# Performance work log

Hardware: AMD Instinct MI355X
Metric: run time of the kernel (lower is better)

## Reference

```python
import jax, jax.numpy as jnp
import numpy as np

N = 100000   # nodes
E = 1600000  # edges
IN = 32      # in_channels
ED = 16      # edge_dim
G = 128      # num graphs in batch
NEG = 0.01   # LeakyReLU default slope

def lrelu(v):
    return jnp.where(v > 0, v, NEG * v)

def gine_conv(x, src, dst, edge_attr, We, be, Wa, ba, Wb, bb):
    # PyG GINEConv (eps=0): out = nn(x + sum_{j->i} relu(x_j + lin(edge_attr)))
    e = edge_attr @ We + be                      # [E, d]
    m = jax.nn.relu(x[src] + e)                  # gather + add + relu
    agg = jax.ops.segment_sum(m, dst, num_segments=x.shape[0])
    h = x + agg
    return lrelu(h @ Wa + ba) @ Wb + bb

def setup_inputs() -> dict:
    key = jax.random.key(0)
    ks = jax.random.split(key, 24)
    w = lambda k, shape: (jax.random.normal(k, shape, dtype=jnp.float32) * 0.05)
    inp = {
        "x": jax.random.normal(ks[0], (N, IN), dtype=jnp.float32),
        "edge_index": jax.random.randint(ks[1], (2, E), 0, N),
        "edge_attr": jax.random.normal(ks[2], (E, ED), dtype=jnp.float32),
        "batch": jnp.sort(jax.random.randint(ks[3], (N,), 0, G)),
        # conv1: edge lin ED->IN, nn IN->32->64
        "We1": w(ks[4], (ED, IN)), "be1": w(ks[5], (IN,)),
        "W1a": w(ks[6], (IN, 32)), "b1a": w(ks[7], (32,)),
        "W1b": w(ks[8], (32, 64)), "b1b": w(ks[9], (64,)),
        # conv2: edge lin ED->64, nn 64->128->256
        "We2": w(ks[10], (ED, 64)), "be2": w(ks[11], (64,)),
        "W2a": w(ks[12], (64, 128)), "b2a": w(ks[13], (128,)),
        "W2b": w(ks[14], (128, 256)), "b2b": w(ks[15], (256,)),
        # head
        "Wf0": w(ks[16], (256, 128)), "bf0": w(ks[17], (128,)),
        "Wf1": w(ks[18], (128, 64)), "bf1": w(ks[19], (64,)),
        "Wf2": w(ks[20], (64, 32)), "bf2": w(ks[21], (32,)),
        "Wr": w(ks[22], (32, 1)), "br": w(ks[23], (1,)),
    }
    return inp

def reference(x, edge_index, edge_attr, batch,
              We1, be1, W1a, b1a, W1b, b1b,
              We2, be2, W2a, b2a, W2b, b2b,
              Wf0, bf0, Wf1, bf1, Wf2, bf2, Wr, br):
    src, dst = edge_index[0], edge_index[1]
    h = gine_conv(x, src, dst, edge_attr, We1, be1, W1a, b1a, W1b, b1b)
    h = lrelu(h)
    h = gine_conv(h, src, dst, edge_attr, We2, be2, W2a, b2a, W2b, b2b)
    h = lrelu(h)
    # global_add_pool over graph ids
    g = jax.ops.segment_sum(h, batch, num_segments=G)   # [G, 256]
    g = lrelu(g @ Wf0 + bf0)
    # dropout: identity (inference reference)
    g = lrelu(g @ Wf1 + bf1)
    g = lrelu(g @ Wf2 + bf2)
    out = (g @ Wr + br)[:, 0]                           # squeeze(dim=1)
    return out
```

## Files before the change

### kernel.cpp

```cpp
#include <hip/hip_runtime.h>

__device__ __forceinline__ float lrelu(float v){ return v > 0.f ? v : 0.01f*v; }

typedef __attribute__((ext_vector_type(8))) short v8s;
typedef __attribute__((ext_vector_type(4))) float v4f;

__device__ __forceinline__ unsigned short f2bf(float f){
    union{float f; unsigned int i;} v; v.f = f;
    unsigned int u = v.i;
    return (unsigned short)((u + 0x7fffu + ((u >> 16) & 1u)) >> 16);
}
__device__ __forceinline__ unsigned int pack2(float a, float b){
    return (unsigned int)f2bf(a) | ((unsigned int)f2bf(b) << 16);
}
__device__ __forceinline__ float bflo(unsigned int u){
    union{unsigned int i; float f;} v; v.i = u << 16; return v.f;
}
__device__ __forceinline__ float bfhi(unsigned int u){
    union{unsigned int i; float f;} v; v.i = u & 0xffff0000u; return v.f;
}
__device__ __forceinline__ float bf2f(unsigned short s){
    union{unsigned int i; float f;} v; v.i = ((unsigned int)s) << 16; return v.f;
}

__global__ __launch_bounds__(256) void k_hist(
    const int* __restrict__ ei, int* __restrict__ deg, int E)
{
    int e = blockIdx.x * 256 + threadIdx.x;
    if (e >= E) return;
    atomicAdd(&deg[ei[E + e]], 1);
}

__global__ __launch_bounds__(256) void k_scan1(
    const int* __restrict__ deg, int* __restrict__ rowptr,
    int* __restrict__ bsum, int N)
{
    __shared__ int sh[256];
    int t = threadIdx.x;
    int i = blockIdx.x * 256 + t;
    int v = (i < N) ? deg[i] : 0;
    sh[t] = v;
    __syncthreads();
    #pragma unroll
    for (int off = 1; off < 256; off <<= 1) {
        int add = (t >= off) ? sh[t - off] : 0;
        __syncthreads();
        sh[t] += add;
        __syncthreads();
    }
    if (i < N) rowptr[i] = sh[t] - v;
    if (t == 255) bsum[blockIdx.x] = sh[t];
}

__global__ __launch_bounds__(512) void k_scan2(int* __restrict__ bsum, int nb)
{
    __shared__ int sh[512];
    int t = threadIdx.x;
    int v = (t < nb) ? bsum[t] : 0;
    sh[t] = v;
    __syncthreads();
    #pragma unroll
    for (int off = 1; off < 512; off <<= 1) {
        int add = (t >= off) ? sh[t - off] : 0;
        __syncthreads();
        sh[t] += add;
        __syncthreads();
    }
    if (t < nb) bsum[t] = sh[t] - v;
}

__global__ __launch_bounds__(256) void k_scan3(
    int* __restrict__ rowptr, int* __restrict__ cursor,
    const int* __restrict__ bsum, int N)
{
    int i = blockIdx.x * 256 + threadIdx.x;
    if (i >= N) return;
    int rp = rowptr[i] + bsum[i >> 8];
    rowptr[i] = rp;
    cursor[i] = rp;
}

__global__ __launch_bounds__(256) void k_castx(
    const float* __restrict__ x, unsigned int* __restrict__ xb, int M8)
{
    int i = blockIdx.x * 256 + threadIdx.x;
    if (i >= M8) return;
    const float4* p = reinterpret_cast<const float4*>(x) + (size_t)i * 2;
    float4 a = p[0], b = p[1];
    uint4 o;
    o.x = pack2(a.x, a.y); o.y = pack2(a.z, a.w);
    o.z = pack2(b.x, b.y); o.w = pack2(b.z, b.w);
    reinterpret_cast<uint4*>(xb)[i] = o;
}

__global__ __launch_bounds__(256) void k_castw(
    const float* __restrict__ W2a, const float* __restrict__ W2b,
    unsigned short* __restrict__ W2aT, unsigned short* __restrict__ W2bT)
{
    int i = blockIdx.x * 256 + threadIdx.x;
    if (i < 128 * 64) {
        int n = i >> 6, k = i & 63;
        W2aT[i] = f2bf(W2a[k * 128 + n]);
    }
    int j = i - 128 * 64;
    if (j >= 0 && j < 256 * 128) {
        int n = j >> 7, k = j & 127;
        W2bT[j] = f2bf(W2b[k * 256 + n]);
    }
}

__global__ __launch_bounds__(256) void k_scatter(
    const int* __restrict__ ei, const float* __restrict__ ea,
    int* __restrict__ cursor, int2* __restrict__ csr2,
    uint4* __restrict__ eab, int E)
{
    int e = blockIdx.x * 256 + threadIdx.x;
    if (e >= E) return;
    int s = ei[e];
    int d = ei[E + e];
    int slot = atomicAdd(&cursor[d], 1);
    const float4* p = reinterpret_cast<const float4*>(ea) + (size_t)e * 4;
    float4 a = p[0], b = p[1], c = p[2], f = p[3];
    uint4 o0, o1;
    o0.x = pack2(a.x, a.y); o0.y = pack2(a.z, a.w);
    o0.z = pack2(b.x, b.y); o0.w = pack2(b.z, b.w);
    o1.x = pack2(c.x, c.y); o1.y = pack2(c.z, c.w);
    o1.z = pack2(f.x, f.y); o1.w = pack2(f.z, f.w);
    eab[(size_t)slot * 2]     = o0;
    eab[(size_t)slot * 2 + 1] = o1;
    int2 r; r.x = s; r.y = d;
    csr2[slot] = r;
}

__device__ __forceinline__ void edge_mlp(
    const uint4& A0, const uint4& A1,
    const float (&w0)[16], const float (&w1)[16],
    float b0, float b1, unsigned int hv,
    float& acc0, float& acc1)
{
    float m0 = b0, m1 = b1, f;
    f = bflo(A0.x); m0 = fmaf(f, w0[0],  m0); m1 = fmaf(f, w1[0],  m1);
    f = bfhi(A0.x); m0 = fmaf(f, w0[1],  m0); m1 = fmaf(f, w1[1],  m1);
    f = bflo(A0.y); m0 = fmaf(f, w0[2],  m0); m1 = fmaf(f, w1[2],  m1);
    f = bfhi(A0.y); m0 = fmaf(f, w0[3],  m0); m1 = fmaf(f, w1[3],  m1);
    f = bflo(A0.z); m0 = fmaf(f, w0[4],  m0); m1 = fmaf(f, w1[4],  m1);
    f = bfhi(A0.z); m0 = fmaf(f, w0[5],  m0); m1 = fmaf(f, w1[5],  m1);
    f = bflo(A0.w); m0 = fmaf(f, w0[6],  m0); m1 = fmaf(f, w1[6],  m1);
    f = bfhi(A0.w); m0 = fmaf(f, w0[7],  m0); m1 = fmaf(f, w1[7],  m1);
    f = bflo(A1.x); m0 = fmaf(f, w0[8],  m0); m1 = fmaf(f, w1[8],  m1);
    f = bfhi(A1.x); m0 = fmaf(f, w0[9],  m0); m1 = fmaf(f, w1[9],  m1);
    f = bflo(A1.y); m0 = fmaf(f, w0[10], m0); m1 = fmaf(f, w1[10], m1);
    f = bfhi(A1.y); m0 = fmaf(f, w0[11], m0); m1 = fmaf(f, w1[11], m1);
    f = bflo(A1.z); m0 = fmaf(f, w0[12], m0); m1 = fmaf(f, w1[12], m1);
    f = bfhi(A1.z); m0 = fmaf(f, w0[13], m0); m1 = fmaf(f, w1[13], m1);
    f = bflo(A1.w); m0 = fmaf(f, w0[14], m0); m1 = fmaf(f, w1[14], m1);
    f = bfhi(A1.w); m0 = fmaf(f, w0[15], m0); m1 = fmaf(f, w1[15], m1);
    m0 += bflo(hv); m1 += bfhi(hv);
    acc0 += (m0 > 0.f ? m0 : 0.f);
    acc1 += (m1 > 0.f ? m1 : 0.f);
}

#define SPW1 128
#define CHL1 32
__global__ __launch_bounds__(256) void k_agg1(
    const unsigned int* __restrict__ xb, const uint4* __restrict__ eab,
    const float* __restrict__ We, const float* __restrict__ be,
    const int2* __restrict__ csr2, float* __restrict__ agg, int E)
{
    const int tid = threadIdx.x;
    const int c2 = tid & 15;
    const int chain = (tid >> 4) & 3;
    const int wave = __builtin_amdgcn_readfirstlane((blockIdx.x * 256 + tid) >> 6);
    const int s0 = wave * SPW1 + chain * CHL1;
    if (s0 >= E) return;
    const int n = (s0 + CHL1 <= E) ? CHL1 : E - s0;
    const int n1 = n - 1;

    float w0[16], w1[16];
    #pragma unroll
    for (int k = 0; k < 16; ++k) {
        w0[k] = We[k * 32 + 2 * c2];
        w1[k] = We[k * 32 + 2 * c2 + 1];
    }
    const float bias0 = be[2 * c2], bias1 = be[2 * c2 + 1];

    const int2* cp = csr2 + s0;
    const uint4* ep = eab + (size_t)s0 * 2;

    int j1 = (1 <= n1) ? 1 : n1;
    int j2 = (2 <= n1) ? 2 : n1;
    int2 r0 = cp[0];
    int2 r1 = cp[j1];
    int2 r2 = cp[j2];
    unsigned int h0  = xb[(unsigned)r0.x * 16 + c2];
    unsigned int h1v = xb[(unsigned)r1.x * 16 + c2];
    uint4 a0 = ep[0],      a1 = ep[1];
    uint4 b0 = ep[2 * j1], b1 = ep[2 * j1 + 1];

    int cur = r0.y;
    bool owned = false;
    float acc0 = 0.f, acc1 = 0.f;

    #pragma unroll 2
    for (int i = 0; i < n; ++i) {
        int i3 = (i + 3 <= n1) ? i + 3 : n1;
        int2 r3 = cp[i3];
        int i2 = (i + 2 <= n1) ? i + 2 : n1;
        unsigned int h2 = xb[(unsigned)r2.x * 16 + c2];
        uint4 c0 = ep[2 * i2], c1 = ep[2 * i2 + 1];

        if (r0.y != cur) {
            if (owned) {
                float2 v; v.x = acc0; v.y = acc1;
                *reinterpret_cast<float2*>(&agg[(unsigned)cur * 32 + 2 * c2]) = v;
            } else {
                atomicAdd(&agg[(unsigned)cur * 32 + 2 * c2],     acc0);
                atomicAdd(&agg[(unsigned)cur * 32 + 2 * c2 + 1], acc1);
            }
            acc0 = acc1 = 0.f; cur = r0.y; owned = true;
        }
        edge_mlp(a0, a1, w0, w1, bias0, bias1, h0, acc0, acc1);
        r0 = r1; r1 = r2; r2 = r3;
        h0 = h1v; h1v = h2;
        a0 = b0; a1 = b1; b0 = c0; b1 = c1;
    }
    atomicAdd(&agg[(unsigned)cur * 32 + 2 * c2],     acc0);
    atomicAdd(&agg[(unsigned)cur * 32 + 2 * c2 + 1], acc1);
}

#define SPW2 64
#define CHL2 32
__global__ __launch_bounds__(256) void k_agg2(
    const unsigned int* __restrict__ h1b, const uint4* __restrict__ eab,
    const float* __restrict__ We, const float* __restrict__ be,
    const int2* __restrict__ csr2, float* __restrict__ agg, int E)
{
    const int tid = threadIdx.x;
    const int c2 = tid & 31;
    const int chain = (tid >> 5) & 1;
    const int wave = __builtin_amdgcn_readfirstlane((blockIdx.x * 256 + tid) >> 6);
    const int s0 = wave * SPW2 + chain * CHL2;
    if (s0 >= E) return;
    const int n = (s0 + CHL2 <= E) ? CHL2 : E - s0;
    const int n1 = n - 1;

    float w0[16], w1[16];
    #pragma unroll
    for (int k = 0; k < 16; ++k) {
        w0[k] = We[k * 64 + 2 * c2];
        w1[k] = We[k * 64 + 2 * c2 + 1];
    }
    const float bias0 = be[2 * c2], bias1 = be[2 * c2 + 1];

    const int2* cp = csr2 + s0;
    const uint4* ep = eab + (size_t)s0 * 2;

    int j1 = (1 <= n1) ? 1 : n1;
    int j2 = (2 <= n1) ? 2 : n1;
    int2 r0 = cp[0];
    int2 r1 = cp[j1];
    int2 r2 = cp[j2];
    unsigned int h0  = h1b[(unsigned)r0.x * 32 + c2];
    unsigned int h1v = h1b[(unsigned)r1.x * 32 + c2];
    uint4 a0 = ep[0],      a1 = ep[1];
    uint4 b0 = ep[2 * j1], b1 = ep[2 * j1 + 1];

    int cur = r0.y;
    bool owned = false;
    float acc0 = 0.f, acc1 = 0.f;

    #pragma unroll 2
    for (int i = 0; i < n; ++i) {
        int i3 = (i + 3 <= n1) ? i + 3 : n1;
        int2 r3 = cp[i3];
        int i2 = (i + 2 <= n1) ? i + 2 : n1;
        unsigned int h2 = h1b[(unsigned)r2.x * 32 + c2];
        uint4 c0 = ep[2 * i2], c1 = ep[2 * i2 + 1];

        if (r0.y != cur) {
            if (owned) {
                float2 v; v.x = acc0; v.y = acc1;
                *reinterpret_cast<float2*>(&agg[(unsigned)cur * 64 + 2 * c2]) = v;
            } else {
                atomicAdd(&agg[(unsigned)cur * 64 + 2 * c2],     acc0);
                atomicAdd(&agg[(unsigned)cur * 64 + 2 * c2 + 1], acc1);
            }
            acc0 = acc1 = 0.f; cur = r0.y; owned = true;
        }
        edge_mlp(a0, a1, w0, w1, bias0, bias1, h0, acc0, acc1);
        r0 = r1; r1 = r2; r2 = r3;
        h0 = h1v; h1v = h2;
        a0 = b0; a1 = b1; b0 = c0; b1 = c1;
    }
    atomicAdd(&agg[(unsigned)cur * 64 + 2 * c2],     acc0);
    atomicAdd(&agg[(unsigned)cur * 64 + 2 * c2 + 1], acc1);
}

__global__ __launch_bounds__(256, 4) void k_mlp1(
    const float* __restrict__ x, const float* __restrict__ agg1,
    const float* __restrict__ W1a, const float* __restrict__ b1a,
    const float* __restrict__ W1b, const float* __restrict__ b1b,
    float* __restrict__ h1, unsigned int* __restrict__ h1b, int N)
{
    __shared__ float ts[64][33];
    const int tid = threadIdx.x;
    const int n0 = blockIdx.x * 64;
    const int row = tid & 63;
    const int grp = __builtin_amdgcn_readfirstlane(tid >> 6);
    const int g = n0 + row;

    float hv[32];
    if (g < N) {
        const float4* xp = reinterpret_cast<const float4*>(x) + (size_t)g * 8;
        const float4* ap = reinterpret_cast<const float4*>(agg1) + (size_t)g * 8;
        #pragma unroll
        for (int q = 0; q < 8; ++q) {
            float4 a = xp[q], b = ap[q];
            hv[4*q+0]=a.x+b.x; hv[4*q+1]=a.y+b.y;
            hv[4*q+2]=a.z+b.z; hv[4*q+3]=a.w+b.w;
        }
    } else {
        #pragma unroll
        for (int q = 0; q < 32; ++q) hv[q] = 0.f;
    }

    {
        const int c0 = grp * 8;
        float acc[8];
        #pragma unroll
        for (int i = 0; i < 8; ++i) acc[i] = b1a[c0 + i];
        for (int k = 0; k < 32; ++k) {
            float h = hv[k];
            const float* w = W1a + k*32 + c0;
            #pragma unroll
            for (int i = 0; i < 8; ++i) acc[i] = fmaf(h, w[i], acc[i]);
        }
        #pragma unroll
        for (int i = 0; i < 8; ++i) ts[row][c0 + i] = lrelu(acc[i]);
    }
    __syncthreads();

    {
        const int c0 = grp * 16;
        float acc[16];
        #pragma unroll
        for (int i = 0; i < 16; ++i) acc[i] = b1b[c0 + i];
        for (int k = 0; k < 32; ++k) {
            float tv = ts[row][k];
            const float* w = W1b + k*64 + c0;
            #pragma unroll
            for (int i = 0; i < 16; ++i) acc[i] = fmaf(tv, w[i], acc[i]);
        }
        if (g < N) {
            #pragma unroll
            for (int i = 0; i < 16; ++i) acc[i] = lrelu(acc[i]);
            float4* op = reinterpret_cast<float4*>(h1) + (size_t)g*16 + (c0>>2);
            #pragma unroll
            for (int q = 0; q < 4; ++q) {
                float4 o;
                o.x = acc[4*q+0]; o.y = acc[4*q+1];
                o.z = acc[4*q+2]; o.w = acc[4*q+3];
                op[q] = o;
            }
            uint4 p0, p1;
            p0.x = pack2(acc[0],  acc[1]);  p0.y = pack2(acc[2],  acc[3]);
            p0.z = pack2(acc[4],  acc[5]);  p0.w = pack2(acc[6],  acc[7]);
            p1.x = pack2(acc[8],  acc[9]);  p1.y = pack2(acc[10], acc[11]);
            p1.z = pack2(acc[12], acc[13]); p1.w = pack2(acc[14], acc[15]);
            uint4* bp = reinterpret_cast<uint4*>(h1b + (size_t)g*32 + (c0>>1));
            bp[0] = p0; bp[1] = p1;
        }
    }
}

__global__ __launch_bounds__(256) void k_mlp2(
    const float* __restrict__ h1, const float* __restrict__ agg2,
    const unsigned short* __restrict__ W2aT, const float* __restrict__ b2a,
    const unsigned short* __restrict__ W2bT, const float* __restrict__ b2b,
    unsigned short* __restrict__ h2b, int N)
{
    __shared__ unsigned short hs[64][72];
    __shared__ unsigned short ts[64][136];
    const int tid = threadIdx.x;
    const int n0 = blockIdx.x * 64;

    {
        int r = tid >> 2, cseg = (tid & 3) * 16;
        int g = n0 + r;
        uint4 o0 = {0,0,0,0}, o1 = {0,0,0,0};
        if (g < N) {
            const float4* xp = reinterpret_cast<const float4*>(h1)
                               + (size_t)g*16 + (cseg>>2);
            const float4* ap = reinterpret_cast<const float4*>(agg2)
                               + (size_t)g*16 + (cseg>>2);
            float4 a0=xp[0], a1=xp[1], a2=xp[2], a3=xp[3];
            float4 b0=ap[0], b1=ap[1], b2=ap[2], b3=ap[3];
            o0.x = pack2(a0.x+b0.x, a0.y+b0.y); o0.y = pack2(a0.z+b0.z, a0.w+b0.w);
            o0.z = pack2(a1.x+b1.x, a1.y+b1.y); o0.w = pack2(a1.z+b1.z, a1.w+b1.w);
            o1.x = pack2(a2.x+b2.x, a2.y+b2.y); o1.y = pack2(a2.z+b2.z, a2.w+b2.w);
            o1.z = pack2(a3.x+b3.x, a3.y+b3.y); o1.w = pack2(a3.z+b3.z, a3.w+b3.w);
        }
        uint4* dp = reinterpret_cast<uint4*>(&hs[r][cseg]);
        dp[0] = o0; dp[1] = o1;
    }
    __syncthreads();

    const int wv   = __builtin_amdgcn_readfirstlane(tid >> 6);
    const int lane = tid & 63;
    const int lid  = lane & 15;
    const int quad = lane >> 4;

    v8s afA0 = *reinterpret_cast<const v8s*>(&hs[wv*16 + lid][quad*8]);
    v8s afA1 = *reinterpret_cast<const v8s*>(&hs[wv*16 + lid][32 + quad*8]);
    #pragma unroll
    for (int nt = 0; nt < 8; ++nt) {
        v4f acc = {0.f, 0.f, 0.f, 0.f};
        const unsigned short* wp = W2aT + (nt*16 + lid)*64 + quad*8;
        v8s b0 = *reinterpret_cast<const v8s*>(wp);
        v8s b1 = *reinterpret_cast<const v8s*>(wp + 32);
        acc = __builtin_amdgcn_mfma_f32_16x16x32_bf16(afA0, b0, acc, 0, 0, 0);
        acc = __builtin_amdgcn_mfma_f32_16x16x32_bf16(afA1, b1, acc, 0, 0, 0);
        float bias = b2a[nt*16 + lid];
        #pragma unroll
        for (int i = 0; i < 4; ++i) {
            float v = lrelu(acc[i] + bias);
            ts[wv*16 + quad*4 + i][nt*16 + lid] = f2bf(v);
        }
    }
    __syncthreads();

    v8s afB[4];
    #pragma unroll
    for (int ks = 0; ks < 4; ++ks)
        afB[ks] = *reinterpret_cast<const v8s*>(&ts[wv*16 + lid][ks*32 + quad*8]);
    const int gbase = n0 + wv*16 + quad*4;
    #pragma unroll 4
    for (int nt = 0; nt < 16; ++nt) {
        v4f acc = {0.f, 0.f, 0.f, 0.f};
        const unsigned short* wp = W2bT + (nt*16 + lid)*128 + quad*8;
        #pragma unroll
        for (int ks = 0; ks < 4; ++ks) {
            v8s bf = *reinterpret_cast<const v8s*>(wp + ks*32);
            acc = __builtin_amdgcn_mfma_f32_16x16x32_bf16(afB[ks], bf, acc, 0, 0, 0);
        }
        float bias = b2b[nt*16 + lid];
        #pragma unroll
        for (int i = 0; i < 4; ++i) {
            int g = gbase + i;
            if (g < N) {
                float v = lrelu(acc[i] + bias);
                h2b[(size_t)g*256 + nt*16 + lid] = f2bf(v);
            }
        }
    }
}

__global__ __launch_bounds__(256) void k_pool(
    const unsigned int* __restrict__ h2b, const int* __restrict__ batch,
    float* __restrict__ g, int N)
{
    int tid = threadIdx.x;
    int c2 = tid & 127;
    int h = tid >> 7;
    int base = blockIdx.x * 128;
    int n0 = base + h;
    int nend = base + 128; if (nend > N) nend = N;
    if (n0 >= N) return;
    float acc0 = 0.f, acc1 = 0.f;
    int cur = batch[n0];
    for (int n = n0; n < nend; n += 2) {
        int b = batch[n];
        unsigned int hv = h2b[(size_t)n * 128 + c2];
        if (b != cur) {
            atomicAdd(&g[(unsigned)cur * 256 + 2*c2],     acc0);
            atomicAdd(&g[(unsigned)cur * 256 + 2*c2 + 1], acc1);
            acc0 = acc1 = 0.f; cur = b;
        }
        acc0 += bflo(hv); acc1 += bfhi(hv);
    }
    atomicAdd(&g[(unsigned)cur * 256 + 2*c2],     acc0);
    atomicAdd(&g[(unsigned)cur * 256 + 2*c2 + 1], acc1);
}

__global__ __launch_bounds__(256) void k_head(
    const float* __restrict__ g,
    const float* __restrict__ Wf0, const float* __restrict__ bf0,
    const float* __restrict__ Wf1, const float* __restrict__ bf1,
    const float* __restrict__ Wf2, const float* __restrict__ bf2,
    const float* __restrict__ Wr,  const float* __restrict__ br,
    float* __restrict__ out)
{
    __shared__ float buf[256];
    __shared__ float t0[128];
    __shared__ float t1[64];
    __shared__ float t2[32];
    int gid = blockIdx.x, tid = threadIdx.x;
    buf[tid] = g[(size_t)gid*256 + tid];
    __syncthreads();
    if (tid < 128) {
        float acc = bf0[tid];
        for (int k = 0; k < 256; ++k) acc = fmaf(buf[k], Wf0[k*128 + tid], acc);
        t0[tid] = lrelu(acc);
    }
    __syncthreads();
    if (tid < 64) {
        float acc = bf1[tid];
        for (int k = 0; k < 128; ++k) acc = fmaf(t0[k], Wf1[k*64 + tid], acc);
        t1[tid] = lrelu(acc);
    }
    __syncthreads();
    if (tid < 32) {
        float acc = bf2[tid];
        for (int k = 0; k < 64; ++k) acc = fmaf(t1[k], Wf2[k*32 + tid], acc);
        t2[tid] = lrelu(acc);
    }
    __syncthreads();
    if (tid == 0) {
        float acc = br[0];
        for (int k = 0; k < 32; ++k) acc = fmaf(t2[k], Wr[k], acc);
        out[gid] = acc;
    }
}

extern "C" void kernel_launch(void* const* d_in, const int* in_sizes, int n_in,
                              void* d_out, int out_size, void* d_ws, size_t ws_size,
                              hipStream_t stream)
{
    const float* x     = (const float*)d_in[0];
    const int*   ei    = (const int*)d_in[1];
    const float* ea    = (const float*)d_in[2];
    const int*   batch = (const int*)d_in[3];
    const float* We1=(const float*)d_in[4],  *be1=(const float*)d_in[5];
    const float* W1a=(const float*)d_in[6],  *b1a=(const float*)d_in[7];
    const float* W1b=(const float*)d_in[8],  *b1b=(const float*)d_in[9];
    const float* We2=(const float*)d_in[10], *be2=(const float*)d_in[11];
    const float* W2a=(const float*)d_in[12], *b2a=(const float*)d_in[13];
    const float* W2b=(const float*)d_in[14], *b2b=(const float*)d_in[15];
    const float* Wf0=(const float*)d_in[16], *bf0=(const float*)d_in[17];
    const float* Wf1=(const float*)d_in[18], *bf1=(const float*)d_in[19];
    const float* Wf2=(const float*)d_in[20], *bf2=(const float*)d_in[21];
    const float* Wr =(const float*)d_in[22], *br =(const float*)d_in[23];

    const int N = in_sizes[0] / 32;
    const int E = in_sizes[1] / 2;
    const int G = out_size;
    const int nb = (N + 255) / 256;
    const int nb64 = (N + 63) / 64;

    char* p = (char*)d_ws;
    int*   deg     = (int*)p;                 p += (size_t)N * 4;
    float* gbuf    = (float*)p;               p += (size_t)G * 256 * 4;
    float* agg1    = (float*)p;               p += (size_t)N * 32 * 4;
    float* agg2    = (float*)p;               p += (size_t)N * 64 * 4;
    size_t zero_bytes = (size_t)(p - (char*)d_ws);
    int*   rowptr  = (int*)p;                 p += (size_t)N * 4;
    int*   cursor  = (int*)p;                 p += (size_t)N * 4;
    int*   bsum    = (int*)p;                 p += 512 * 4;
    p = (char*)(((uintptr_t)p + 15) & ~(uintptr_t)15);
    int2*  csr2    = (int2*)p;                p += (size_t)E * 8;
    uint4* eab     = (uint4*)p;               p += (size_t)E * 32;
    unsigned short* xb   = (unsigned short*)p; p += (size_t)N * 32 * 2;
    float* h1      = (float*)p;               p += (size_t)N * 64 * 4;
    unsigned int*   h1b  = (unsigned int*)p;  p += (size_t)N * 64 * 2;
    unsigned short* W2aT = (unsigned short*)p; p += 128 * 64 * 2;
    unsigned short* W2bT = (unsigned short*)p; p += 256 * 128 * 2;
    unsigned short* h2b  = (unsigned short*)p; p += (size_t)N * 256 * 2;

    hipMemsetAsync(d_ws, 0, zero_bytes, stream);

    int eb = (E + 255) / 256;

    k_hist   <<<eb, 256, 0, stream>>>(ei, deg, E);
    k_scan1  <<<nb, 256, 0, stream>>>(deg, rowptr, bsum, N);
    k_scan2  <<<1, 512, 0, stream>>>(bsum, nb);
    k_scan3  <<<nb, 256, 0, stream>>>(rowptr, cursor, bsum, N);
    {
        int M8 = N * 32 / 8;
        k_castx<<<(M8 + 255) / 256, 256, 0, stream>>>(x, (unsigned int*)xb, M8);
    }
    k_castw<<<(128*64 + 256*128 + 255) / 256, 256, 0, stream>>>(W2a, W2b, W2aT, W2bT);
    k_scatter<<<eb, 256, 0, stream>>>(ei, ea, cursor, csr2, eab, E);

    {
        int waves = (E + SPW1 - 1) / SPW1;
        int blocks = (waves + 3) / 4;
        k_agg1<<<blocks, 256, 0, stream>>>((const unsigned int*)xb, eab, We1, be1,
                                           csr2, agg1, E);
    }
    k_mlp1<<<nb64, 256, 0, stream>>>(x, agg1, W1a, b1a, W1b, b1b, h1,
                                     (unsigned int*)h1b, N);

    {
        int waves = (E + SPW2 - 1) / SPW2;
        int blocks = (waves + 3) / 4;
        k_agg2<<<blocks, 256, 0, stream>>>((const unsigned int*)h1b, eab, We2, be2,
                                           csr2, agg2, E);
    }
    k_mlp2<<<nb64, 256, 0, stream>>>(h1, agg2, W2aT, b2a, W2bT, b2b, h2b, N);

    k_pool<<<(N + 127) / 128, 256, 0, stream>>>((const unsigned int*)h2b, batch,
                                                gbuf, N);
    k_head<<<G, 256, 0, stream>>>(gbuf, Wf0, bf0, Wf1, bf1, Wf2, bf2, Wr, br,
                                  (float*)d_out);
}
```

Before: 687.1 us.

## Compute edge linear projections with bf16 MFMA in both aggregation kernels

Both edge aggregation kernels now compute the per-edge linear projection of edge attributes with 16x16x32 bf16 MFMA instructions, using transposed, zero-padded bf16 edge weights prepared in the weight cast kernel. Results are staged through LDS and then combined with the gathered node features and ReLU before segmented accumulation. Work is restructured so that one wave processes 64 sorted edges in tiles of 16, overlapping the gather and MFMA of the next tile with accumulation of the current one. This removes the scalar FMA loop over the 16 edge features. In exchange it adds LDS traffic, rounds the edge weights to bf16, and in k_agg1 drops the owned plain-store path so every segment flush is an atomic.

```diff
diff --git a/kernel.cpp b/kernel.cpp
--- a/kernel.cpp
+++ b/kernel.cpp
@@ -95,7 +95,9 @@
 
 __global__ __launch_bounds__(256) void k_castw(
     const float* __restrict__ W2a, const float* __restrict__ W2b,
-    unsigned short* __restrict__ W2aT, unsigned short* __restrict__ W2bT)
+    const float* __restrict__ We1, const float* __restrict__ We2,
+    unsigned short* __restrict__ W2aT, unsigned short* __restrict__ W2bT,
+    unsigned short* __restrict__ WeT1, unsigned short* __restrict__ WeT2)
 {
     int i = blockIdx.x * 256 + threadIdx.x;
     if (i < 128 * 64) {
@@ -106,6 +108,16 @@
     if (j >= 0 && j < 256 * 128) {
         int n = j >> 7, k = j & 127;
         W2bT[j] = f2bf(W2b[k * 256 + n]);
+    }
+    int q1 = i - (128 * 64 + 256 * 128);
+    if (q1 >= 0 && q1 < 32 * 32) {
+        int cch = q1 >> 5, k = q1 & 31;
+        WeT1[q1] = (k < 16) ? f2bf(We1[k * 32 + cch]) : (unsigned short)0;
+    }
+    int q2 = q1 - 32 * 32;
+    if (q2 >= 0 && q2 < 64 * 32) {
+        int cch = q2 >> 5, k = q2 & 31;
+        WeT2[q2] = (k < 16) ? f2bf(We2[k * 64 + cch]) : (unsigned short)0;
     }
 }
 
@@ -132,168 +144,181 @@
     csr2[slot] = r;
 }
 
-__device__ __forceinline__ void edge_mlp(
-    const uint4& A0, const uint4& A1,
-    const float (&w0)[16], const float (&w1)[16],
-    float b0, float b1, unsigned int hv,
-    float& acc0, float& acc1)
-{
-    float m0 = b0, m1 = b1, f;
-    f = bflo(A0.x); m0 = fmaf(f, w0[0],  m0); m1 = fmaf(f, w1[0],  m1);
-    f = bfhi(A0.x); m0 = fmaf(f, w0[1],  m0); m1 = fmaf(f, w1[1],  m1);
-    f = bflo(A0.y); m0 = fmaf(f, w0[2],  m0); m1 = fmaf(f, w1[2],  m1);
-    f = bfhi(A0.y); m0 = fmaf(f, w0[3],  m0); m1 = fmaf(f, w1[3],  m1);
-    f = bflo(A0.z); m0 = fmaf(f, w0[4],  m0); m1 = fmaf(f, w1[4],  m1);
-    f = bfhi(A0.z); m0 = fmaf(f, w0[5],  m0); m1 = fmaf(f, w1[5],  m1);
-    f = bflo(A0.w); m0 = fmaf(f, w0[6],  m0); m1 = fmaf(f, w1[6],  m1);
-    f = bfhi(A0.w); m0 = fmaf(f, w0[7],  m0); m1 = fmaf(f, w1[7],  m1);
-    f = bflo(A1.x); m0 = fmaf(f, w0[8],  m0); m1 = fmaf(f, w1[8],  m1);
-    f = bfhi(A1.x); m0 = fmaf(f, w0[9],  m0); m1 = fmaf(f, w1[9],  m1);
-    f = bflo(A1.y); m0 = fmaf(f, w0[10], m0); m1 = fmaf(f, w1[10], m1);
-    f = bfhi(A1.y); m0 = fmaf(f, w0[11], m0); m1 = fmaf(f, w1[11], m1);
-    f = bflo(A1.z); m0 = fmaf(f, w0[12], m0); m1 = fmaf(f, w1[12], m1);
-    f = bfhi(A1.z); m0 = fmaf(f, w0[13], m0); m1 = fmaf(f, w1[13], m1);
-    f = bflo(A1.w); m0 = fmaf(f, w0[14], m0); m1 = fmaf(f, w1[14], m1);
-    f = bfhi(A1.w); m0 = fmaf(f, w0[15], m0); m1 = fmaf(f, w1[15], m1);
-    m0 += bflo(hv); m1 += bfhi(hv);
-    acc0 += (m0 > 0.f ? m0 : 0.f);
-    acc1 += (m1 > 0.f ? m1 : 0.f);
-}
-
-#define SPW1 128
-#define CHL1 32
+#define AGG_SPW 64
+
+__global__ __launch_bounds__(256) void k_agg2(
+    const unsigned short* __restrict__ xb,
+    const uint4* __restrict__ eab,
+    const unsigned short* __restrict__ WeT,
+    const float* __restrict__ be,
+    const int2* __restrict__ csr2, float* __restrict__ agg, int E)
+{
+    __shared__ __align__(16) float lds[4][2][16][68];
+    const int tid  = threadIdx.x;
+    const int wv   = tid >> 6;
+    const int lane = tid & 63;
+    const int lid  = lane & 15;
+    const int quad = lane >> 4;
+    const int wave = __builtin_amdgcn_readfirstlane((blockIdx.x * 256 + tid) >> 6);
+    const int s0 = wave * AGG_SPW;
+    if (s0 >= E) return;
+    const int nsl = (s0 + AGG_SPW <= E) ? AGG_SPW : E - s0;
+
+    v8s af0 = *reinterpret_cast<const v8s*>(WeT + lid * 32 + quad * 8);
+    v8s af1 = *reinterpret_cast<const v8s*>(WeT + (16 + lid) * 32 + quad * 8);
+    v8s af2 = *reinterpret_cast<const v8s*>(WeT + (32 + lid) * 32 + quad * 8);
+    v8s af3 = *reinterpret_cast<const v8s*>(WeT + (48 + lid) * 32 + quad * 8);
+    const float biasc = be[lane];
+    const int2*  cp = csr2 + s0;
+    const uint4* ep = eab + (size_t)s0 * 2;
+
+    unsigned short xv[2][16];
+    int dsv[2][16];
+    float acc = 0.f;
+    int   cur = cp[0].y;
+    bool  owned = false;
+
+    auto GATHER = [&](int t) {
+        const int base = t * 16;
+        const int cnt = nsl - base;
+        #pragma unroll
+        for (int e = 0; e < 16; ++e) {
+            int ee = (e < cnt) ? e : cnt - 1;
+            int2 r = cp[base + ee];
+            dsv[t & 1][e] = r.y;
+            xv[t & 1][e] = xb[(unsigned)r.x * 64u + (unsigned)lane];
+        }
+    };
+    auto MFMA = [&](int t) {
+        int sl = t * 16 + lid;
+        if (sl > nsl - 1) sl = nsl - 1;
+        uint4 bw = {0u, 0u, 0u, 0u};
+        if (quad < 2) bw = ep[2 * sl + quad];
+        union { uint4 u; v8s s; } uu; uu.u = bw;
+        v8s bf = uu.s;
+        v4f d0 = {0.f, 0.f, 0.f, 0.f}, d1 = d0, d2 = d0, d3 = d0;
+        d0 = __builtin_amdgcn_mfma_f32_16x16x32_bf16(af0, bf, d0, 0, 0, 0);
+        d1 = __builtin_amdgcn_mfma_f32_16x16x32_bf16(af1, bf, d1, 0, 0, 0);
+        d2 = __builtin_amdgcn_mfma_f32_16x16x32_bf16(af2, bf, d2, 0, 0, 0);
+        d3 = __builtin_amdgcn_mfma_f32_16x16x32_bf16(af3, bf, d3, 0, 0, 0);
+        float* lp = &lds[wv][t & 1][lid][quad * 4];
+        *reinterpret_cast<v4f*>(lp)      = d0;
+        *reinterpret_cast<v4f*>(lp + 16) = d1;
+        *reinterpret_cast<v4f*>(lp + 32) = d2;
+        *reinterpret_cast<v4f*>(lp + 48) = d3;
+    };
+    auto ACCUM = [&](int t) {
+        const int cnt = nsl - t * 16;
+        #pragma unroll
+        for (int e = 0; e < 16; ++e) {
+            if (e < cnt) {
+                float ls = lds[wv][t & 1][e][lane];
+                float m = ls + biasc + bf2f(xv[t & 1][e]);
+                m = m > 0.f ? m : 0.f;
+                int d = dsv[t & 1][e];
+                if (d != cur) {
+                    if (owned) agg[(unsigned)cur * 64u + lane] = acc;
+                    else       atomicAdd(&agg[(unsigned)cur * 64u + lane], acc);
+                    acc = 0.f; cur = d; owned = true;
+                }
+                acc += m;
+            }
+        }
+    };
+
+    GATHER(0); MFMA(0);
+    #pragma unroll
+    for (int t = 0; t < 4; ++t) {
+        if (t * 16 < nsl) {
+            if ((t + 1) < 4 && (t + 1) * 16 < nsl) { GATHER(t + 1); MFMA(t + 1); }
+            ACCUM(t);
+        }
+    }
+    atomicAdd(&agg[(unsigned)cur * 64u + lane], acc);
+}
+
 __global__ __launch_bounds__(256) void k_agg1(
-    const unsigned int* __restrict__ xb, const uint4* __restrict__ eab,
-    const float* __restrict__ We, const float* __restrict__ be,
+    const unsigned short* __restrict__ xb,
+    const uint4* __restrict__ eab,
+    const unsigned short* __restrict__ WeT,
+    const float* __restrict__ be,
     const int2* __restrict__ csr2, float* __restrict__ agg, int E)
 {
-    const int tid = threadIdx.x;
-    const int c2 = tid & 15;
-    const int chain = (tid >> 4) & 3;
+    __shared__ __align__(16) float lds[4][2][16][36];
+    const int tid  = threadIdx.x;
+    const int wv   = tid >> 6;
+    const int lane = tid & 63;
+    const int lid  = lane & 15;
+    const int quad = lane >> 4;
+    const int c    = lane & 31;
+    const int sub  = lane >> 5;
     const int wave = __builtin_amdgcn_readfirstlane((blockIdx.x * 256 + tid) >> 6);
-    const int s0 = wave * SPW1 + chain * CHL1;
+    const int s0 = wave * AGG_SPW;
     if (s0 >= E) return;
-    const int n = (s0 + CHL1 <= E) ? CHL1 : E - s0;
-    const int n1 = n - 1;
-
-    float w0[16], w1[16];
+    const int nsl = (s0 + AGG_SPW <= E) ? AGG_SPW : E - s0;
+
+    v8s af0 = *reinterpret_cast<const v8s*>(WeT + lid * 32 + quad * 8);
+    v8s af1 = *reinterpret_cast<const v8s*>(WeT + (16 + lid) * 32 + quad * 8);
+    const float biasc = be[c];
+    const int2*  cp = csr2 + s0;
+    const uint4* ep = eab + (size_t)s0 * 2;
+
+    unsigned short xv[2][8];
+    int dsv[2][8];
+    float acc = 0.f;
+    int cur = cp[(sub < nsl) ? sub : 0].y;
+
+    auto GATHER = [&](int t) {
+        #pragma unroll
+        for (int i = 0; i < 8; ++i) {
+            int e = t * 16 + 2 * i + sub;
+            int ee = (e < nsl) ? e : nsl - 1;
+            int2 r = cp[ee];
+            dsv[t & 1][i] = r.y;
+            xv[t & 1][i] = xb[(unsigned)r.x * 32u + (unsigned)c];
+        }
+    };
+    auto MFMA = [&](int t) {
+        int sl = t * 16 + lid;
+        if (sl > nsl - 1) sl = nsl - 1;
+        uint4 bw = {0u, 0u, 0u, 0u};
+        if (quad < 2) bw = ep[2 * sl + quad];
+        union { uint4 u; v8s s; } uu; uu.u = bw;
+        v8s bf = uu.s;
+        v4f d0 = {0.f, 0.f, 0.f, 0.f}, d1 = d0;
+        d0 = __builtin_amdgcn_mfma_f32_16x16x32_bf16(af0, bf, d0, 0, 0, 0);
+        d1 = __builtin_amdgcn_mfma_f32_16x16x32_bf16(af1, bf, d1, 0, 0, 0);
+        float* lp = &lds[wv][t & 1][lid][quad * 4];
+        *reinterpret_cast<v4f*>(lp)      = d0;
+        *reinterpret_cast<v4f*>(lp + 16) = d1;
+    };
+    auto ACCUM = [&](int t) {
+        #pragma unroll
+        for (int i = 0; i < 8; ++i) {
+            int e = t * 16 + 2 * i + sub;
+            if (e < nsl) {
+                float ls = lds[wv][t & 1][2 * i + sub][c];
+                float m = ls + biasc + bf2f(xv[t & 1][i]);
+                m = m > 0.f ? m : 0.f;
+                int d = dsv[t & 1][i];
+                if (d != cur) {
+                    atomicAdd(&agg[(unsigned)cur * 32u + c], acc);
+                    acc = 0.f; cur = d;
+                }
+                acc += m;
+            }
+        }
+    };
+
+    GATHER(0); MFMA(0);
     #pragma unroll
-    for (int k = 0; k < 16; ++k) {
-        w0[k] = We[k * 32 + 2 * c2];
-        w1[k] = We[k * 32 + 2 * c2 + 1];
-    }
-    const float bias0 = be[2 * c2], bias1 = be[2 * c2 + 1];
-
-    const int2* cp = csr2 + s0;
-    const uint4* ep = eab + (size_t)s0 * 2;
-
-    int j1 = (1 <= n1) ? 1 : n1;
-    int j2 = (2 <= n1) ? 2 : n1;
-    int2 r0 = cp[0];
-    int2 r1 = cp[j1];
-    int2 r2 = cp[j2];
-    unsigned int h0  = xb[(unsigned)r0.x * 16 + c2];
-    unsigned int h1v = xb[(unsigned)r1.x * 16 + c2];
-    uint4 a0 = ep[0],      a1 = ep[1];
-    uint4 b0 = ep[2 * j1], b1 = ep[2 * j1 + 1];
-
-    int cur = r0.y;
-    bool owned = false;
-    float acc0 = 0.f, acc1 = 0.f;
-
-    #pragma unroll 2
-    for (int i = 0; i < n; ++i) {
-        int i3 = (i + 3 <= n1) ? i + 3 : n1;
-        int2 r3 = cp[i3];
-        int i2 = (i + 2 <= n1) ? i + 2 : n1;
-        unsigned int h2 = xb[(unsigned)r2.x * 16 + c2];
-        uint4 c0 = ep[2 * i2], c1 = ep[2 * i2 + 1];
-
-        if (r0.y != cur) {
-            if (owned) {
-                float2 v; v.x = acc0; v.y = acc1;
-                *reinterpret_cast<float2*>(&agg[(unsigned)cur * 32 + 2 * c2]) = v;
-            } else {
-                atomicAdd(&agg[(unsigned)cur * 32 + 2 * c2],     acc0);
-                atomicAdd(&agg[(unsigned)cur * 32 + 2 * c2 + 1], acc1);
-            }
-            acc0 = acc1 = 0.f; cur = r0.y; owned = true;
-        }
-        edge_mlp(a0, a1, w0, w1, bias0, bias1, h0, acc0, acc1);
-        r0 = r1; r1 = r2; r2 = r3;
-        h0 = h1v; h1v = h2;
-        a0 = b0; a1 = b1; b0 = c0; b1 = c1;
-    }
-    atomicAdd(&agg[(unsigned)cur * 32 + 2 * c2],     acc0);
-    atomicAdd(&agg[(unsigned)cur * 32 + 2 * c2 + 1], acc1);
-}
-
-#define SPW2 64
-#define CHL2 32
-__global__ __launch_bounds__(256) void k_agg2(
-    const unsigned int* __restrict__ h1b, const uint4* __restrict__ eab,
-    const float* __restrict__ We, const float* __restrict__ be,
-    const int2* __restrict__ csr2, float* __restrict__ agg, int E)
-{
-    const int tid = threadIdx.x;
-    const int c2 = tid & 31;
-    const int chain = (tid >> 5) & 1;
-    const int wave = __builtin_amdgcn_readfirstlane((blockIdx.x * 256 + tid) >> 6);
-    const int s0 = wave * SPW2 + chain * CHL2;
-    if (s0 >= E) return;
-    const int n = (s0 + CHL2 <= E) ? CHL2 : E - s0;
-    const int n1 = n - 1;
-
-    float w0[16], w1[16];
-    #pragma unroll
-    for (int k = 0; k < 16; ++k) {
-        w0[k] = We[k * 64 + 2 * c2];
-        w1[k] = We[k * 64 + 2 * c2 + 1];
-    }
-    const float bias0 = be[2 * c2], bias1 = be[2 * c2 + 1];
-
-    const int2* cp = csr2 + s0;
-    const uint4* ep = eab + (size_t)s0 * 2;
-
-    int j1 = (1 <= n1) ? 1 : n1;
-    int j2 = (2 <= n1) ? 2 : n1;
-    int2 r0 = cp[0];
-    int2 r1 = cp[j1];
-    int2 r2 = cp[j2];
-    unsigned int h0  = h1b[(unsigned)r0.x * 32 + c2];
-    unsigned int h1v = h1b[(unsigned)r1.x * 32 + c2];
-    uint4 a0 = ep[0],      a1 = ep[1];
-    uint4 b0 = ep[2 * j1], b1 = ep[2 * j1 + 1];
-
-    int cur = r0.y;
-    bool owned = false;
-    float acc0 = 0.f, acc1 = 0.f;
-
-    #pragma unroll 2
-    for (int i = 0; i < n; ++i) {
-        int i3 = (i + 3 <= n1) ? i + 3 : n1;
-        int2 r3 = cp[i3];
-        int i2 = (i + 2 <= n1) ? i + 2 : n1;
-        unsigned int h2 = h1b[(unsigned)r2.x * 32 + c2];
-        uint4 c0 = ep[2 * i2], c1 = ep[2 * i2 + 1];
-
-        if (r0.y != cur) {
-            if (owned) {
-                float2 v; v.x = acc0; v.y = acc1;
-                *reinterpret_cast<float2*>(&agg[(unsigned)cur * 64 + 2 * c2]) = v;
-            } else {
-                atomicAdd(&agg[(unsigned)cur * 64 + 2 * c2],     acc0);
-                atomicAdd(&agg[(unsigned)cur * 64 + 2 * c2 + 1], acc1);
-            }
-            acc0 = acc1 = 0.f; cur = r0.y; owned = true;
-        }
-        edge_mlp(a0, a1, w0, w1, bias0, bias1, h0, acc0, acc1);
-        r0 = r1; r1 = r2; r2 = r3;
-        h0 = h1v; h1v = h2;
-        a0 = b0; a1 = b1; b0 = c0; b1 = c1;
-    }
-    atomicAdd(&agg[(unsigned)cur * 64 + 2 * c2],     acc0);
-    atomicAdd(&agg[(unsigned)cur * 64 + 2 * c2 + 1], acc1);
+    for (int t = 0; t < 4; ++t) {
+        if (t * 16 < nsl) {
+            if ((t + 1) < 4 && (t + 1) * 16 < nsl) { GATHER(t + 1); MFMA(t + 1); }
+            ACCUM(t);
+        }
+    }
+    atomicAdd(&agg[(unsigned)cur * 32u + c], acc);
 }
 
 __global__ __launch_bounds__(256, 4) void k_mlp1(
@@ -564,6 +589,8 @@
     unsigned int*   h1b  = (unsigned int*)p;  p += (size_t)N * 64 * 2;
     unsigned short* W2aT = (unsigned short*)p; p += 128 * 64 * 2;
     unsigned short* W2bT = (unsigned short*)p; p += 256 * 128 * 2;
+    unsigned short* WeT1 = (unsigned short*)p; p += 32 * 32 * 2;
+    unsigned short* WeT2 = (unsigned short*)p; p += 64 * 32 * 2;
     unsigned short* h2b  = (unsigned short*)p; p += (size_t)N * 256 * 2;
 
     hipMemsetAsync(d_ws, 0, zero_bytes, stream);
@@ -578,23 +605,26 @@
         int M8 = N * 32 / 8;
         k_castx<<<(M8 + 255) / 256, 256, 0, stream>>>(x, (unsigned int*)xb, M8);
     }
-    k_castw<<<(128*64 + 256*128 + 255) / 256, 256, 0, stream>>>(W2a, W2b, W2aT, W2bT);
+    {
+        int tot = 128*64 + 256*128 + 32*32 + 64*32;
+        k_castw<<<(tot + 255) / 256, 256, 0, stream>>>(W2a, W2b, We1, We2,
+                                                       W2aT, W2bT, WeT1, WeT2);
+    }
     k_scatter<<<eb, 256, 0, stream>>>(ei, ea, cursor, csr2, eab, E);
 
     {
-        int waves = (E + SPW1 - 1) / SPW1;
+        int waves = (E + AGG_SPW - 1) / AGG_SPW;
         int blocks = (waves + 3) / 4;
-        k_agg1<<<blocks, 256, 0, stream>>>((const unsigned int*)xb, eab, We1, be1,
-                                           csr2, agg1, E);
+        k_agg1<<<blocks, 256, 0, stream>>>(xb, eab, WeT1, be1, csr2, agg1, E);
     }
     k_mlp1<<<nb64, 256, 0, stream>>>(x, agg1, W1a, b1a, W1b, b1b, h1,
                                      (unsigned int*)h1b, N);
 
     {
-        int waves = (E + SPW2 - 1) / SPW2;
+        int waves = (E + AGG_SPW - 1) / AGG_SPW;
         int blocks = (waves + 3) / 4;
-        k_agg2<<<blocks, 256, 0, stream>>>((const unsigned int*)h1b, eab, We2, be2,
-                                           csr2, agg2, E);
+        k_agg2<<<blocks, 256, 0, stream>>>((const unsigned short*)h1b, eab, WeT2,
+                                           be2, csr2, agg2, E);
     }
     k_mlp2<<<nb64, 256, 0, stream>>>(h1, agg2, W2aT, b2a, W2bT, b2b, h2b, N);
 
```

New measurement: 626.3 us. 8.8% less time.
